# Kernel tuning notes

Measured on AMD Instinct MI355X. Metric: run time of the kernel, lower is better.

Reference implementation:

```python
import jax, jax.numpy as jnp
import numpy as np

NUM_GROUPS = 32
EPS = 1e-6


def group_norm(x, gamma, beta):
    # x: [B, C, H, W]
    B, C, H, W = x.shape
    xg = x.reshape(B, NUM_GROUPS, C // NUM_GROUPS, H, W)
    mean = jnp.mean(xg, axis=(2, 3, 4), keepdims=True)
    var = jnp.var(xg, axis=(2, 3, 4), keepdims=True)
    xn = ((xg - mean) * jax.lax.rsqrt(var + EPS)).reshape(B, C, H, W)
    return xn * gamma[None, :, None, None] + beta[None, :, None, None]


def conv1x1(x, w, b):
    # x: [B, C, H, W], w: [O, C], b: [O]  (1x1 conv == channel matmul)
    return jnp.einsum('oc,bchw->bohw', w, x) + b[None, :, None, None]


def setup_inputs() -> dict:
    key = jax.random.key(0)
    ks = jax.random.split(key, 10)
    B, C, H, W = 16, 512, 32, 32
    s = 1.0 / np.sqrt(C)
    inp = {
        'hidden_states': jax.random.normal(ks[0], (B, C, H, W), dtype=jnp.float32),
        'norm_gamma': jnp.ones((C,), dtype=jnp.float32),
        'norm_beta': jnp.zeros((C,), dtype=jnp.float32),
        'wq': jax.random.normal(ks[1], (C, C), dtype=jnp.float32) * s,
        'bq': jnp.zeros((C,), dtype=jnp.float32),
        'wk': jax.random.normal(ks[2], (C, C), dtype=jnp.float32) * s,
        'bk': jnp.zeros((C,), dtype=jnp.float32),
        'wv': jax.random.normal(ks[3], (C, C), dtype=jnp.float32) * s,
        'bv': jnp.zeros((C,), dtype=jnp.float32),
        'wo': jax.random.normal(ks[4], (C, C), dtype=jnp.float32) * s,
        'bo': jnp.zeros((C,), dtype=jnp.float32),
    }
    return inp


def reference(hidden_states, norm_gamma, norm_beta, wq, bq, wk, bk, wv, bv, wo, bo):
    residual = hidden_states
    h = group_norm(hidden_states, norm_gamma, norm_beta)
    q = conv1x1(h, wq, bq)  # [B, C, H, W]
    k = conv1x1(h, wk, bk)
    v = conv1x1(h, wv, bv)
    B, C, H, W = q.shape
    N = H * W
    qf = q.reshape(B, C, N)  # [B, C, N]
    kf = k.reshape(B, C, N)
    vf = v.reshape(B, C, N)
    scale = float(C) ** (-0.5)
    # attn_weights[b, i, j] = sum_c q[b,c,i] * k[b,c,j]
    attn = jnp.einsum('bci,bcj->bij', qf, kf) * scale
    attn = jax.nn.softmax(attn, axis=2)
    # out[b, c, i] = sum_j v[b,c,j] * attn[b,i,j]
    out = jnp.einsum('bcj,bij->bci', vf, attn).reshape(B, C, H, W)
    out = conv1x1(out, wo, bo)
    return residual + out
```

## Files before the change

kernel.cpp:

```cpp
#include <hip/hip_runtime.h>

typedef __attribute__((ext_vector_type(4))) float f32x4;
typedef __attribute__((ext_vector_type(8))) __bf16 bf16x8;
typedef __attribute__((ext_vector_type(4))) unsigned short us4;
typedef __attribute__((ext_vector_type(8))) unsigned short us8;

#define B_  16
#define C_  512
#define N_  1024
#define G_  32
#define GS  16

__device__ inline unsigned short f2bf(float f) {
  unsigned u = __builtin_bit_cast(unsigned, f);
  u += 0x7fffu + ((u >> 16) & 1u);
  return (unsigned short)(u >> 16);
}
__device__ inline float bf2f(unsigned short u) {
  unsigned x = (unsigned)u << 16;
  return __builtin_bit_cast(float, x);
}

#define GLOAD_LDS16(gp, lp) __builtin_amdgcn_global_load_lds( \
    (const __attribute__((address_space(1))) unsigned int*)(gp), \
    (__attribute__((address_space(3))) unsigned int*)(lp), 16, 0, 0)

__global__ __launch_bounds__(256) void gn_stats(const float* __restrict__ x,
                                                float* __restrict__ stats) {
  int bg = blockIdx.x;
  const float* xp = x + (long)bg * (GS * N_);
  int tid = threadIdx.x;
  float s = 0.f, ss = 0.f;
  for (int i = tid * 4; i < GS * N_; i += 1024) {
    f32x4 v = *(const f32x4*)&xp[i];
    s += v.x + v.y + v.z + v.w;
    ss += v.x * v.x + v.y * v.y + v.z * v.z + v.w * v.w;
  }
  __shared__ float r1[256], r2[256];
  r1[tid] = s; r2[tid] = ss; __syncthreads();
  for (int off = 128; off > 0; off >>= 1) {
    if (tid < off) { r1[tid] += r1[tid + off]; r2[tid] += r2[tid + off]; }
    __syncthreads();
  }
  if (tid == 0) {
    float mean = r1[0] * (1.f / (GS * N_));
    float var  = r2[0] * (1.f / (GS * N_)) - mean * mean;
    stats[bg * 2]     = mean;
    stats[bg * 2 + 1] = rsqrtf(var + 1e-6f);
  }
}

__global__ __launch_bounds__(256) void gn_apply(const float* __restrict__ x,
                                                const float* __restrict__ stats,
                                                const float* __restrict__ gamma,
                                                const float* __restrict__ beta,
                                                unsigned short* __restrict__ ht) {
  int b = blockIdx.z, ct = blockIdx.y, nt = blockIdx.x;
  int c0 = ct * 64, n0 = nt * 64;
  int tid = threadIdx.x;
  __shared__ unsigned short L[64 * 68];
  const float* xp = x + ((long)b * C_ + c0) * N_ + n0;
#pragma unroll
  for (int i = 0; i < 4; ++i) {
    int li = tid + i * 256;
    int row = li >> 4;
    int col4 = (li & 15) * 4;
    f32x4 v = *(const f32x4*)&xp[(long)row * N_ + col4];
    int c = c0 + row;
    float mean = stats[(b * G_ + (c >> 4)) * 2];
    float rstd = stats[(b * G_ + (c >> 4)) * 2 + 1];
    float gm = gamma[c] * rstd;
    float bt = beta[c] - mean * gm;
    us4 o;
    o.x = f2bf(v.x * gm + bt); o.y = f2bf(v.y * gm + bt);
    o.z = f2bf(v.z * gm + bt); o.w = f2bf(v.w * gm + bt);
    *(us4*)&L[row * 68 + col4] = o;
  }
  __syncthreads();
#pragma unroll
  for (int i = 0; i < 2; ++i) {
    int s = tid + i * 256;
    int n = s >> 3;
    int cs = (s & 7) * 8;
    us8 o;
#pragma unroll
    for (int j = 0; j < 8; ++j) o[j] = L[(cs + j) * 68 + n];
    *(us8*)&ht[((long)b * N_ + n0 + n) * C_ + c0 + cs] = o;
  }
}

__global__ __launch_bounds__(256) void convert_w(const float* __restrict__ wo,
                                                 const float* __restrict__ bv,
                                                 unsigned short* __restrict__ wob,
                                                 float* __restrict__ bvo) {
  long bid = blockIdx.x;
  int tid = threadIdx.x;
  long i = bid * 256 + tid;
  if (i < C_ * C_) wob[i] = f2bf(wo[i]);
  if (bid >= 1024) {
    int o = (int)(bid - 1024) * 256 + tid;
    const float* wr = wo + (long)o * 512;
    float acc = 0.f;
    for (int c = 0; c < 512; c += 4) {
      f32x4 w4 = *(const f32x4*)&wr[c];
      f32x4 b4 = *(const f32x4*)&bv[c];
      acc += w4.x * b4.x + w4.y * b4.y + w4.z * b4.z + w4.w * b4.w;
    }
    bvo[o] = acc;
  }
}

__global__ __launch_bounds__(256) void transpose3(const float* __restrict__ wq,
                                                  const float* __restrict__ wk,
                                                  const float* __restrict__ wv,
                                                  unsigned short* __restrict__ wqT,
                                                  unsigned short* __restrict__ wkT,
                                                  unsigned short* __restrict__ wvT) {
  const float* src = (blockIdx.z == 0) ? wq : (blockIdx.z == 1) ? wk : wv;
  unsigned short* dst = (blockIdx.z == 0) ? wqT : (blockIdx.z == 1) ? wkT : wvT;
  int c0 = blockIdx.x * 64, k0 = blockIdx.y * 64;
  int tid = threadIdx.x;
  __shared__ float Lt[64][65];
#pragma unroll
  for (int i = 0; i < 4; ++i) {
    int lin = tid + i * 256;
    int rr = lin >> 4;
    int q4 = (lin & 15) * 4;
    f32x4 v = *(const f32x4*)&src[(long)(c0 + rr) * 512 + k0 + q4];
    Lt[q4 + 0][rr] = v.x; Lt[q4 + 1][rr] = v.y;
    Lt[q4 + 2][rr] = v.z; Lt[q4 + 3][rr] = v.w;
  }
  __syncthreads();
#pragma unroll
  for (int i = 0; i < 2; ++i) {
    int lin = tid + i * 256;
    int kk = lin >> 3;
    int cc = (lin & 7) * 8;
    us8 o;
#pragma unroll
    for (int j = 0; j < 8; ++j) o[j] = f2bf(Lt[kk][cc + j]);
    *(us8*)&dst[(long)(k0 + kk) * 512 + c0 + cc] = o;
  }
}

__device__ inline f32x4 mfma16(bf16x8 a, bf16x8 b, f32x4 c) {
  return __builtin_amdgcn_mfma_f32_16x16x32_bf16(a, b, c, 0, 0, 0);
}

__global__ __launch_bounds__(256) void wprod(const unsigned short* __restrict__ wkT,
                                             const unsigned short* __restrict__ wqT,
                                             const unsigned short* __restrict__ wob,
                                             const unsigned short* __restrict__ wvT,
                                             unsigned short* __restrict__ WM,
                                             unsigned short* __restrict__ WVO) {
  const unsigned short* A = blockIdx.z ? wob : wkT;
  const unsigned short* B = blockIdx.z ? wvT : wqT;
  unsigned short* D = blockIdx.z ? WVO : WM;
  int row0 = blockIdx.x * 64, col0 = blockIdx.y * 64;
  int tid = threadIdx.x, lane = tid & 63, w = tid >> 6;
  int lr = lane & 15, kh = (lane >> 4) * 8;
  f32x4 acc4[4];
#pragma unroll
  for (int n = 0; n < 4; ++n) acc4[n] = f32x4{0.f, 0.f, 0.f, 0.f};
  for (int k0 = 0; k0 < 512; k0 += 32) {
    bf16x8 af = *(const bf16x8*)&A[(long)(row0 + w * 16 + lr) * 512 + k0 + kh];
#pragma unroll
    for (int n = 0; n < 4; ++n) {
      bf16x8 bf8 = *(const bf16x8*)&B[(long)(col0 + n * 16 + lr) * 512 + k0 + kh];
      acc4[n] = mfma16(af, bf8, acc4[n]);
    }
  }
  int rb = (lane >> 4) * 4;
#pragma unroll
  for (int n = 0; n < 4; ++n)
#pragma unroll
    for (int r = 0; r < 4; ++r)
      D[(long)(row0 + w * 16 + rb + r) * 512 + col0 + n * 16 + lr] = f2bf(acc4[n][r]);
}

__global__ __launch_bounds__(256) void uv_kernel(const unsigned short* __restrict__ wqT,
                                                 const unsigned short* __restrict__ wkT,
                                                 const float* __restrict__ bq,
                                                 const float* __restrict__ bk,
                                                 float* __restrict__ u, float* __restrict__ v,
                                                 float* __restrict__ s0g) {
  int tid = threadIdx.x, lane = tid & 63, wv_ = tid >> 6;
  int gw = blockIdx.x * 4 + wv_;
  int half = gw >> 5;
  const unsigned short* W = half ? wkT : wqT;
  const float* bvec = half ? bq : bk;
  f32x4 b4a = *(const f32x4*)&bvec[lane * 8];
  f32x4 b4b = *(const f32x4*)&bvec[lane * 8 + 4];
  for (int rr = 0; rr < 16; ++rr) {
    int row = (gw & 31) * 16 + rr;
    us8 w8 = *(const us8*)&W[(long)row * 512 + lane * 8];
    float d = bf2f(w8[0]) * b4a.x + bf2f(w8[1]) * b4a.y + bf2f(w8[2]) * b4a.z + bf2f(w8[3]) * b4a.w
            + bf2f(w8[4]) * b4b.x + bf2f(w8[5]) * b4b.y + bf2f(w8[6]) * b4b.z + bf2f(w8[7]) * b4b.w;
#pragma unroll
    for (int off = 1; off < 64; off <<= 1) d += __shfl_xor(d, off);
    if (lane == 0) { if (half) v[row] = d; else u[row] = d; }
  }
  if (gw == 0) {
    f32x4 qa = *(const f32x4*)&bq[lane * 8];
    f32x4 qb = *(const f32x4*)&bq[lane * 8 + 4];
    f32x4 ka = *(const f32x4*)&bk[lane * 8];
    f32x4 kb = *(const f32x4*)&bk[lane * 8 + 4];
    float d = qa.x * ka.x + qa.y * ka.y + qa.z * ka.z + qa.w * ka.w
            + qb.x * kb.x + qb.y * kb.y + qb.z * kb.z + qb.w * kb.w;
#pragma unroll
    for (int off = 1; off < 64; off <<= 1) d += __shfl_xor(d, off);
    if (lane == 0) s0g[0] = d;
  }
}

__global__ __launch_bounds__(256) void alphabeta(const unsigned short* __restrict__ ht,
                                                 const float* __restrict__ u,
                                                 const float* __restrict__ v,
                                                 const float* __restrict__ s0g,
                                                 float* __restrict__ alpha,
                                                 float* __restrict__ betav) {
  int tid = threadIdx.x, lane = tid & 63, w = tid >> 6;
  long gw = (long)blockIdx.x * 4 + w;
  f32x4 ua = *(const f32x4*)&u[lane * 8];
  f32x4 ub = *(const f32x4*)&u[lane * 8 + 4];
  f32x4 va = *(const f32x4*)&v[lane * 8];
  f32x4 vb = *(const f32x4*)&v[lane * 8 + 4];
  float s0 = s0g[0];
  for (int rr = 0; rr < 16; ++rr) {
    long row = gw * 16 + rr;
    us8 h8 = *(const us8*)&ht[row * 512 + lane * 8];
    float h0 = bf2f(h8[0]), h1 = bf2f(h8[1]), h2 = bf2f(h8[2]), h3 = bf2f(h8[3]);
    float h4 = bf2f(h8[4]), h5 = bf2f(h8[5]), h6 = bf2f(h8[6]), h7 = bf2f(h8[7]);
    float du = h0 * ua.x + h1 * ua.y + h2 * ua.z + h3 * ua.w
             + h4 * ub.x + h5 * ub.y + h6 * ub.z + h7 * ub.w;
    float dv = h0 * va.x + h1 * va.y + h2 * va.z + h3 * va.w
             + h4 * vb.x + h5 * vb.y + h6 * vb.z + h7 * vb.w;
#pragma unroll
    for (int off = 1; off < 64; off <<= 1) {
      du += __shfl_xor(du, off);
      dv += __shfl_xor(dv, off);
    }
    if (lane == 0) { alpha[row] = s0 + du; betav[row] = dv; }
  }
}

__device__ inline int swz(int b) { return b ^ (((b >> 9) & 1) << 5); }

template<int NREP, int EPI, int XSWZ>
__global__ __launch_bounds__(512, 2) void gemm256(
    const unsigned short* __restrict__ A, long lda, long Az,
    const unsigned short* __restrict__ Bm, long ldb, long Bz,
    void* __restrict__ Dp, long ldd, long Dz,
    const float* __restrict__ bias, float scale, int K,
    const float* __restrict__ residual, float* __restrict__ rs) {
  constexpr int BN = NREP * 64;
  int bx = blockIdx.x, by = blockIdx.y, bz = blockIdx.z;
  if constexpr (XSWZ) {
    int lin = bx + 4 * (by + 4 * bz);
    int l2  = (lin & 7) * 32 + (lin >> 3);
    bx = l2 & 3; by = (l2 >> 2) & 3; bz = l2 >> 4;
  }
  const int z = bz;
  const long row0 = (long)bx * 256;
  const long col0 = (long)by * BN;
  const int tid  = threadIdx.x;
  const int lane = tid & 63;
  const int wave = tid >> 6;
  const int wm = wave >> 2;
  const int wn = wave & 3;
  const int lr = lane & 15;
  const int khb = (lane >> 4) * 16;

  __shared__ unsigned short Abuf[2][16384];
  __shared__ unsigned short Bbuf[2][NREP * 4096];
  __shared__ float sred[256];

  const unsigned short* Ab = A  + (long)z * Az;
  const unsigned short* Bb = Bm + (long)z * Bz;

  if constexpr (EPI == 7) {
    if (tid < 256) {
      const float* rp = rs + ((long)z * 1024 + row0 + tid) * 16;
      float s = 0.f;
#pragma unroll
      for (int i = 0; i < 16; ++i) s += rp[i];
      sred[tid] = 1.f / s;
    }
    asm volatile("s_waitcnt lgkmcnt(0)" ::: "memory");
  }

  const unsigned short* gA[4];
#pragma unroll
  for (int r = 0; r < 4; ++r) {
    int L = swz(r * 8192 + tid * 16);
    gA[r] = Ab + (row0 + (L >> 7)) * lda + ((L & 127) >> 1);
  }
  const unsigned short* gB[NREP];
#pragma unroll
  for (int r = 0; r < NREP; ++r) {
    int L = swz(r * 8192 + tid * 16);
    gB[r] = Bb + (col0 + (L >> 7)) * ldb + ((L & 127) >> 1);
  }

  f32x4 acc[8][NREP];
#pragma unroll
  for (int m = 0; m < 8; ++m)
#pragma unroll
    for (int n = 0; n < NREP; ++n) acc[m][n] = f32x4{0.f, 0.f, 0.f, 0.f};

  const int NT = K >> 6;
#pragma unroll
  for (int r = 0; r < 4; ++r)    GLOAD_LDS16(gA[r], &Abuf[0][r * 4096 + wave * 512]);
#pragma unroll
  for (int r = 0; r < NREP; ++r) GLOAD_LDS16(gB[r], &Bbuf[0][r * 4096 + wave * 512]);

  for (int t = 0; t < NT; ++t) {
    int tn = t + 1; if (tn == NT) tn = 0;
    const long ko = (long)tn << 6;
    const int nb = (t + 1) & 1;
#pragma unroll
    for (int r = 0; r < 4; ++r)    GLOAD_LDS16(gA[r] + ko, &Abuf[nb][r * 4096 + wave * 512]);
#pragma unroll
    for (int r = 0; r < NREP; ++r) GLOAD_LDS16(gB[r] + ko, &Bbuf[nb][r * 4096 + wave * 512]);
    if constexpr (NREP == 4) asm volatile("s_waitcnt vmcnt(8)" ::: "memory");
    else                     asm volatile("s_waitcnt vmcnt(6)" ::: "memory");
    __builtin_amdgcn_s_barrier();
    __builtin_amdgcn_sched_barrier(0);
    const unsigned short* Al = Abuf[t & 1];
    const unsigned short* Bl = Bbuf[t & 1];
#pragma unroll
    for (int kk = 0; kk < 2; ++kk) {
      bf16x8 af[8], bfr[NREP];
#pragma unroll
      for (int m = 0; m < 8; ++m) {
        int Pb = swz((wm * 128 + m * 16 + lr) * 128 + kk * 64 + khb);
        af[m] = *(const bf16x8*)((const char*)Al + Pb);
      }
#pragma unroll
      for (int n = 0; n < NREP; ++n) {
        int Pb = swz((wn * (NREP * 16) + n * 16 + lr) * 128 + kk * 64 + khb);
        bfr[n] = *(const bf16x8*)((const char*)Bl + Pb);
      }
      __builtin_amdgcn_s_setprio(1);
#pragma unroll
      for (int m = 0; m < 8; ++m)
#pragma unroll
        for (int n = 0; n < NREP; ++n)
          acc[m][n] = mfma16(af[m], bfr[n], acc[m][n]);
      __builtin_amdgcn_s_setprio(0);
    }
    __builtin_amdgcn_sched_barrier(0);
    __builtin_amdgcn_s_barrier();
    __builtin_amdgcn_sched_barrier(0);
  }
  asm volatile("s_waitcnt vmcnt(0)" ::: "memory");
  __builtin_amdgcn_s_barrier();

  const int rb = (lane >> 4) * 4;

  if constexpr (EPI == 7) {
#pragma unroll
    for (int m = 0; m < 8; ++m) {
      int lrow = wm * 128 + m * 16 + rb;
      long gr0 = row0 + lrow;
#pragma unroll
      for (int n = 0; n < NREP; ++n) {
        long gc = col0 + wn * (NREP * 16) + n * 16 + lr;
        long o = (long)z * (512L * 1024L) + gc * 1024L + gr0;
        f32x4 res = *(const f32x4*)&residual[o];
        float bb = bias[gc];
        f32x4 st;
#pragma unroll
        for (int r = 0; r < 4; ++r)
          st[r] = acc[m][n][r] * sred[lrow + r] + bb + res[r];
        *(f32x4*)&((float*)Dp)[o] = st;
      }
    }
    return;
  }

  float* slab = ((float*)(void*)Abuf) + wave * 1088;
  const int jt = by;
  unsigned short* Dst = (unsigned short*)Dp + (long)z * Dz;
  float bc[NREP];
  if constexpr (EPI == 5) {
#pragma unroll
    for (int n = 0; n < NREP; ++n)
      bc[n] = residual[(long)z * 1024 + col0 + wn * (NREP * 16) + n * 16 + lr];
  }
#pragma unroll
  for (int m = 0; m < 8; ++m) {
    float ps[4] = {0.f, 0.f, 0.f, 0.f};
    float ar[4];
    if constexpr (EPI == 5) {
#pragma unroll
      for (int r = 0; r < 4; ++r)
        ar[r] = bias[(long)z * 1024 + row0 + wm * 128 + m * 16 + rb + r];
    }
#pragma unroll
    for (int n = 0; n < NREP; ++n) {
#pragma unroll
      for (int r = 0; r < 4; ++r) {
        float v = acc[m][n][r];
        if constexpr (EPI == 1) v += bias[row0 + wm * 128 + m * 16 + rb + r];
        else if constexpr (EPI == 5) { v = exp2f((v + ar[r] + bc[n]) * scale); ps[r] += v; }
        slab[(rb + r) * 68 + n * 16 + lr] = v;
      }
    }
    if constexpr (EPI == 5) {
#pragma unroll
      for (int r = 0; r < 4; ++r) {
        ps[r] += __shfl_xor(ps[r], 1);
        ps[r] += __shfl_xor(ps[r], 2);
        ps[r] += __shfl_xor(ps[r], 4);
        ps[r] += __shfl_xor(ps[r], 8);
      }
      if (lr == 0) {
#pragma unroll
        for (int r = 0; r < 4; ++r)
          rs[((long)z * 1024 + row0 + wm * 128 + m * 16 + rb + r) * 16 + jt * 4 + wn] = ps[r];
      }
    }
    if constexpr (NREP == 4) {
#pragma unroll
      for (int p = 0; p < 2; ++p) {
        int rl = p * 8 + (lane >> 3);
        int c8 = (lane & 7) * 8;
        f32x4 v0 = *(const f32x4*)&slab[rl * 68 + c8];
        f32x4 v1 = *(const f32x4*)&slab[rl * 68 + c8 + 4];
        us8 o;
        o[0] = f2bf(v0.x); o[1] = f2bf(v0.y); o[2] = f2bf(v0.z); o[3] = f2bf(v0.w);
        o[4] = f2bf(v1.x); o[5] = f2bf(v1.y); o[6] = f2bf(v1.z); o[7] = f2bf(v1.w);
        *(us8*)&Dst[(row0 + wm * 128 + m * 16 + rl) * ldd + col0 + wn * 64 + c8] = o;
      }
    } else {
      int rl = lane >> 2;
      int c8 = (lane & 3) * 8;
      f32x4 v0 = *(const f32x4*)&slab[rl * 68 + c8];
      f32x4 v1 = *(const f32x4*)&slab[rl * 68 + c8 + 4];
      us8 o;
      o[0] = f2bf(v0.x); o[1] = f2bf(v0.y); o[2] = f2bf(v0.z); o[3] = f2bf(v0.w);
      o[4] = f2bf(v1.x); o[5] = f2bf(v1.y); o[6] = f2bf(v1.z); o[7] = f2bf(v1.w);
      *(us8*)&Dst[(row0 + wm * 128 + m * 16 + rl) * ldd + col0 + wn * 32 + c8] = o;
    }
  }
}

extern "C" void kernel_launch(void* const* d_in, const int* in_sizes, int n_in,
                              void* d_out, int out_size, void* d_ws, size_t ws_size,
                              hipStream_t stream) {
  const float* x     = (const float*)d_in[0];
  const float* gamma = (const float*)d_in[1];
  const float* beta  = (const float*)d_in[2];
  const float* wq    = (const float*)d_in[3];
  const float* bq    = (const float*)d_in[4];
  const float* wk    = (const float*)d_in[5];
  const float* bk    = (const float*)d_in[6];
  const float* wv    = (const float*)d_in[7];
  const float* bv    = (const float*)d_in[8];
  const float* wo    = (const float*)d_in[9];
  const float* bo    = (const float*)d_in[10];
  float* out = (float*)d_out;

  char* ws = (char*)d_ws;
  unsigned short* ht   = (unsigned short*)(ws + 0);
  unsigned short* T    = (unsigned short*)(ws + 16777216);
  unsigned short* VWT  = (unsigned short*)(ws + 33554432);
  unsigned short* S    = (unsigned short*)(ws + 50331648);
  unsigned short* wqT  = (unsigned short*)(ws + 83886080);
  unsigned short* wkT  = (unsigned short*)(ws + 84410368);
  unsigned short* wvT  = (unsigned short*)(ws + 84934656);
  unsigned short* wob  = (unsigned short*)(ws + 85458944);
  unsigned short* WM   = (unsigned short*)(ws + 85983232);
  unsigned short* WVO  = (unsigned short*)(ws + 86507520);
  float* u             = (float*)(ws + 87031808);
  float* v             = (float*)(ws + 87033856);
  float* s0g           = (float*)(ws + 87035904);
  float* bvo           = (float*)(ws + 87037952);
  float* stats         = (float*)(ws + 87040000);
  float* alpha         = (float*)(ws + 87046144);
  float* betav         = (float*)(ws + 87111680);
  float* rs            = (float*)(ws + 87177216);

  convert_w<<<1026, 256, 0, stream>>>(wo, bv, wob, bvo);
  transpose3<<<dim3(8, 8, 3), 256, 0, stream>>>(wq, wk, wv, wqT, wkT, wvT);
  wprod<<<dim3(8, 8, 2), 256, 0, stream>>>(wkT, wqT, wob, wvT, WM, WVO);
  uv_kernel<<<16, 256, 0, stream>>>(wqT, wkT, bq, bk, u, v, s0g);
  gn_stats<<<512, 256, 0, stream>>>(x, stats);
  gn_apply<<<dim3(16, 8, 16), 256, 0, stream>>>(x, stats, gamma, beta, ht);
  alphabeta<<<256, 256, 0, stream>>>(ht, u, v, s0g, alpha, betav);

  gemm256<2, 3, 0><<<dim3(64, 4, 1), 512, 0, stream>>>(ht, 512, 0, WM, 512, 0,
                                                       T, 512, 0, nullptr, 0.f, 512, nullptr, nullptr);
  gemm256<2, 1, 0><<<dim3(2, 128, 1), 512, 0, stream>>>(WVO, 512, 0, ht, 512, 0,
                                                        VWT, 16384, 0, bvo, 0.f, 512, nullptr, nullptr);
  gemm256<4, 5, 1><<<dim3(4, 4, 16), 512, 0, stream>>>(T, 512, 524288L, ht, 512, 524288L,
                                                       S, 1024, 1048576L, alpha,
                                                       0.06375871416f, 512, betav, rs);
  gemm256<2, 7, 1><<<dim3(4, 4, 16), 512, 0, stream>>>(S, 1024, 1048576L,
                                                       VWT, 16384, 1024,
                                                       out, 0, 0, bo, 0.f, 1024, x, rs);
}
```

Before: 166.3 us.

## Fuse group-norm stats and apply; shrink GEMM tiles to 128x128 for more blocks

Merges the group-norm statistics and apply kernels into one kernel that stages each group's slice in LDS, so x is read once instead of twice and one launch is removed. All GEMMs switch from 256-row, 512-thread tiles to 128x128 tiles with 256 threads, and the grid swizzle is generalized. This quadruples block counts (e.g. 256 to 1024 for the score GEMM) to fill more CUs, at the cost of less data reuse per tile and more global/L2 traffic. The row-sum partial layout changes to match the new tiling.

```diff
diff --git a/kernel.cpp b/kernel.cpp
--- a/kernel.cpp
+++ b/kernel.cpp
@@ -25,67 +25,49 @@
     (const __attribute__((address_space(1))) unsigned int*)(gp), \
     (__attribute__((address_space(3))) unsigned int*)(lp), 16, 0, 0)
 
-__global__ __launch_bounds__(256) void gn_stats(const float* __restrict__ x,
-                                                float* __restrict__ stats) {
+__global__ __launch_bounds__(256) void gn_fused(const float* __restrict__ x,
+                                                const float* __restrict__ gamma,
+                                                const float* __restrict__ beta,
+                                                unsigned short* __restrict__ ht) {
   int bg = blockIdx.x;
-  const float* xp = x + (long)bg * (GS * N_);
+  int b = bg >> 5, g = bg & 31;
   int tid = threadIdx.x;
+  __shared__ float Lx[16][1028];
+  __shared__ float r1[256], r2[256];
+  const float* xp = x + ((long)b * C_ + g * 16) * N_;
   float s = 0.f, ss = 0.f;
-  for (int i = tid * 4; i < GS * N_; i += 1024) {
-    f32x4 v = *(const f32x4*)&xp[i];
-    s += v.x + v.y + v.z + v.w;
+#pragma unroll
+  for (int i = 0; i < 16; ++i) {
+    f32x4 v = *(const f32x4*)&xp[(long)i * N_ + tid * 4];
+    s  += v.x + v.y + v.z + v.w;
     ss += v.x * v.x + v.y * v.y + v.z * v.z + v.w * v.w;
-  }
-  __shared__ float r1[256], r2[256];
+    *(f32x4*)&Lx[i][tid * 4] = v;
+  }
   r1[tid] = s; r2[tid] = ss; __syncthreads();
   for (int off = 128; off > 0; off >>= 1) {
     if (tid < off) { r1[tid] += r1[tid + off]; r2[tid] += r2[tid + off]; }
     __syncthreads();
   }
-  if (tid == 0) {
-    float mean = r1[0] * (1.f / (GS * N_));
-    float var  = r2[0] * (1.f / (GS * N_)) - mean * mean;
-    stats[bg * 2]     = mean;
-    stats[bg * 2 + 1] = rsqrtf(var + 1e-6f);
-  }
-}
-
-__global__ __launch_bounds__(256) void gn_apply(const float* __restrict__ x,
-                                                const float* __restrict__ stats,
-                                                const float* __restrict__ gamma,
-                                                const float* __restrict__ beta,
-                                                unsigned short* __restrict__ ht) {
-  int b = blockIdx.z, ct = blockIdx.y, nt = blockIdx.x;
-  int c0 = ct * 64, n0 = nt * 64;
-  int tid = threadIdx.x;
-  __shared__ unsigned short L[64 * 68];
-  const float* xp = x + ((long)b * C_ + c0) * N_ + n0;
-#pragma unroll
-  for (int i = 0; i < 4; ++i) {
-    int li = tid + i * 256;
-    int row = li >> 4;
-    int col4 = (li & 15) * 4;
-    f32x4 v = *(const f32x4*)&xp[(long)row * N_ + col4];
-    int c = c0 + row;
-    float mean = stats[(b * G_ + (c >> 4)) * 2];
-    float rstd = stats[(b * G_ + (c >> 4)) * 2 + 1];
-    float gm = gamma[c] * rstd;
-    float bt = beta[c] - mean * gm;
-    us4 o;
-    o.x = f2bf(v.x * gm + bt); o.y = f2bf(v.y * gm + bt);
-    o.z = f2bf(v.z * gm + bt); o.w = f2bf(v.w * gm + bt);
-    *(us4*)&L[row * 68 + col4] = o;
-  }
-  __syncthreads();
-#pragma unroll
-  for (int i = 0; i < 2; ++i) {
-    int s = tid + i * 256;
-    int n = s >> 3;
-    int cs = (s & 7) * 8;
+  float mean = r1[0] * (1.f / 16384.f);
+  float var  = r2[0] * (1.f / 16384.f) - mean * mean;
+  float rstd = rsqrtf(var + 1e-6f);
+  float gm[8], bt[8];
+  int cbase = g * 16 + (tid & 1) * 8;
+#pragma unroll
+  for (int k = 0; k < 8; ++k) {
+    gm[k] = gamma[cbase + k] * rstd;
+    bt[k] = beta[cbase + k] - mean * gm[k];
+  }
+#pragma unroll
+  for (int j = 0; j < 8; ++j) {
+    int lin = tid + j * 256;
+    int n = lin >> 1;
+    int c8 = (lin & 1) * 8;
     us8 o;
 #pragma unroll
-    for (int j = 0; j < 8; ++j) o[j] = L[(cs + j) * 68 + n];
-    *(us8*)&ht[((long)b * N_ + n0 + n) * C_ + c0 + cs] = o;
+    for (int k = 0; k < 8; ++k)
+      o[k] = f2bf(Lx[c8 + k][n] * gm[k] + bt[k]);
+    *(us8*)&ht[((long)b * N_ + n) * C_ + g * 16 + c8] = o;
   }
 }
 
@@ -246,40 +228,42 @@
 
 __device__ inline int swz(int b) { return b ^ (((b >> 9) & 1) << 5); }
 
-template<int NREP, int EPI, int XSWZ>
-__global__ __launch_bounds__(512, 2) void gemm256(
+template<int EPI, int SHX, int SHY, int XSWZ>
+__global__ __launch_bounds__(256, 2) void gemm128(
     const unsigned short* __restrict__ A, long lda, long Az,
     const unsigned short* __restrict__ Bm, long ldb, long Bz,
     void* __restrict__ Dp, long ldd, long Dz,
     const float* __restrict__ bias, float scale, int K,
     const float* __restrict__ residual, float* __restrict__ rs) {
-  constexpr int BN = NREP * 64;
   int bx = blockIdx.x, by = blockIdx.y, bz = blockIdx.z;
   if constexpr (XSWZ) {
-    int lin = bx + 4 * (by + 4 * bz);
-    int l2  = (lin & 7) * 32 + (lin >> 3);
-    bx = l2 & 3; by = (l2 >> 2) & 3; bz = l2 >> 4;
+    int lin = bx + ((by + (bz << SHY)) << SHX);
+    int cpx = 1 << (SHX + SHY + 4 - 3);
+    int l2  = (lin & 7) * cpx + (lin >> 3);
+    bx = l2 & ((1 << SHX) - 1);
+    by = (l2 >> SHX) & ((1 << SHY) - 1);
+    bz = l2 >> (SHX + SHY);
   }
   const int z = bz;
-  const long row0 = (long)bx * 256;
-  const long col0 = (long)by * BN;
+  const long row0 = (long)bx * 128;
+  const long col0 = (long)by * 128;
   const int tid  = threadIdx.x;
   const int lane = tid & 63;
   const int wave = tid >> 6;
-  const int wm = wave >> 2;
-  const int wn = wave & 3;
+  const int wm = wave >> 1;
+  const int wn = wave & 1;
   const int lr = lane & 15;
   const int khb = (lane >> 4) * 16;
 
-  __shared__ unsigned short Abuf[2][16384];
-  __shared__ unsigned short Bbuf[2][NREP * 4096];
-  __shared__ float sred[256];
+  __shared__ unsigned short Abuf[2][8192];
+  __shared__ unsigned short Bbuf[2][8192];
+  __shared__ float sred[128];
 
   const unsigned short* Ab = A  + (long)z * Az;
   const unsigned short* Bb = Bm + (long)z * Bz;
 
   if constexpr (EPI == 7) {
-    if (tid < 256) {
+    if (tid < 128) {
       const float* rp = rs + ((long)z * 1024 + row0 + tid) * 16;
       float s = 0.f;
 #pragma unroll
@@ -290,62 +274,61 @@
   }
 
   const unsigned short* gA[4];
+  const unsigned short* gB[4];
 #pragma unroll
   for (int r = 0; r < 4; ++r) {
-    int L = swz(r * 8192 + tid * 16);
+    int L = swz(r * 4096 + tid * 16);
     gA[r] = Ab + (row0 + (L >> 7)) * lda + ((L & 127) >> 1);
-  }
-  const unsigned short* gB[NREP];
-#pragma unroll
-  for (int r = 0; r < NREP; ++r) {
-    int L = swz(r * 8192 + tid * 16);
     gB[r] = Bb + (col0 + (L >> 7)) * ldb + ((L & 127) >> 1);
   }
 
-  f32x4 acc[8][NREP];
-#pragma unroll
-  for (int m = 0; m < 8; ++m)
-#pragma unroll
-    for (int n = 0; n < NREP; ++n) acc[m][n] = f32x4{0.f, 0.f, 0.f, 0.f};
+  f32x4 acc[4][4];
+#pragma unroll
+  for (int m = 0; m < 4; ++m)
+#pragma unroll
+    for (int n = 0; n < 4; ++n) acc[m][n] = f32x4{0.f, 0.f, 0.f, 0.f};
 
   const int NT = K >> 6;
-#pragma unroll
-  for (int r = 0; r < 4; ++r)    GLOAD_LDS16(gA[r], &Abuf[0][r * 4096 + wave * 512]);
-#pragma unroll
-  for (int r = 0; r < NREP; ++r) GLOAD_LDS16(gB[r], &Bbuf[0][r * 4096 + wave * 512]);
+  const int ldsO = wave * 512;
+
+#pragma unroll
+  for (int r = 0; r < 4; ++r) {
+    GLOAD_LDS16(gA[r], &Abuf[0][r * 2048 + ldsO]);
+    GLOAD_LDS16(gB[r], &Bbuf[0][r * 2048 + ldsO]);
+  }
 
   for (int t = 0; t < NT; ++t) {
     int tn = t + 1; if (tn == NT) tn = 0;
     const long ko = (long)tn << 6;
     const int nb = (t + 1) & 1;
 #pragma unroll
-    for (int r = 0; r < 4; ++r)    GLOAD_LDS16(gA[r] + ko, &Abuf[nb][r * 4096 + wave * 512]);
-#pragma unroll
-    for (int r = 0; r < NREP; ++r) GLOAD_LDS16(gB[r] + ko, &Bbuf[nb][r * 4096 + wave * 512]);
-    if constexpr (NREP == 4) asm volatile("s_waitcnt vmcnt(8)" ::: "memory");
-    else                     asm volatile("s_waitcnt vmcnt(6)" ::: "memory");
+    for (int r = 0; r < 4; ++r) {
+      GLOAD_LDS16(gA[r] + ko, &Abuf[nb][r * 2048 + ldsO]);
+      GLOAD_LDS16(gB[r] + ko, &Bbuf[nb][r * 2048 + ldsO]);
+    }
+    asm volatile("s_waitcnt vmcnt(8)" ::: "memory");
     __builtin_amdgcn_s_barrier();
     __builtin_amdgcn_sched_barrier(0);
     const unsigned short* Al = Abuf[t & 1];
     const unsigned short* Bl = Bbuf[t & 1];
 #pragma unroll
     for (int kk = 0; kk < 2; ++kk) {
-      bf16x8 af[8], bfr[NREP];
-#pragma unroll
-      for (int m = 0; m < 8; ++m) {
-        int Pb = swz((wm * 128 + m * 16 + lr) * 128 + kk * 64 + khb);
+      bf16x8 af[4], bfr[4];
+#pragma unroll
+      for (int m = 0; m < 4; ++m) {
+        int Pb = swz((wm * 64 + m * 16 + lr) * 128 + kk * 64 + khb);
         af[m] = *(const bf16x8*)((const char*)Al + Pb);
       }
 #pragma unroll
-      for (int n = 0; n < NREP; ++n) {
-        int Pb = swz((wn * (NREP * 16) + n * 16 + lr) * 128 + kk * 64 + khb);
+      for (int n = 0; n < 4; ++n) {
+        int Pb = swz((wn * 64 + n * 16 + lr) * 128 + kk * 64 + khb);
         bfr[n] = *(const bf16x8*)((const char*)Bl + Pb);
       }
       __builtin_amdgcn_s_setprio(1);
 #pragma unroll
-      for (int m = 0; m < 8; ++m)
-#pragma unroll
-        for (int n = 0; n < NREP; ++n)
+      for (int m = 0; m < 4; ++m)
+#pragma unroll
+        for (int n = 0; n < 4; ++n)
           acc[m][n] = mfma16(af[m], bfr[n], acc[m][n]);
       __builtin_amdgcn_s_setprio(0);
     }
@@ -360,12 +343,12 @@
 
   if constexpr (EPI == 7) {
 #pragma unroll
-    for (int m = 0; m < 8; ++m) {
-      int lrow = wm * 128 + m * 16 + rb;
+    for (int m = 0; m < 4; ++m) {
+      int lrow = wm * 64 + m * 16 + rb;
       long gr0 = row0 + lrow;
 #pragma unroll
-      for (int n = 0; n < NREP; ++n) {
-        long gc = col0 + wn * (NREP * 16) + n * 16 + lr;
+      for (int n = 0; n < 4; ++n) {
+        long gc = col0 + wn * 64 + n * 16 + lr;
         long o = (long)z * (512L * 1024L) + gc * 1024L + gr0;
         f32x4 res = *(const f32x4*)&residual[o];
         float bb = bias[gc];
@@ -382,27 +365,27 @@
   float* slab = ((float*)(void*)Abuf) + wave * 1088;
   const int jt = by;
   unsigned short* Dst = (unsigned short*)Dp + (long)z * Dz;
-  float bc[NREP];
+  float bc[4];
   if constexpr (EPI == 5) {
 #pragma unroll
-    for (int n = 0; n < NREP; ++n)
-      bc[n] = residual[(long)z * 1024 + col0 + wn * (NREP * 16) + n * 16 + lr];
-  }
-#pragma unroll
-  for (int m = 0; m < 8; ++m) {
+    for (int n = 0; n < 4; ++n)
+      bc[n] = residual[(long)z * 1024 + col0 + wn * 64 + n * 16 + lr];
+  }
+#pragma unroll
+  for (int m = 0; m < 4; ++m) {
     float ps[4] = {0.f, 0.f, 0.f, 0.f};
     float ar[4];
     if constexpr (EPI == 5) {
 #pragma unroll
       for (int r = 0; r < 4; ++r)
-        ar[r] = bias[(long)z * 1024 + row0 + wm * 128 + m * 16 + rb + r];
-    }
-#pragma unroll
-    for (int n = 0; n < NREP; ++n) {
+        ar[r] = bias[(long)z * 1024 + row0 + wm * 64 + m * 16 + rb + r];
+    }
+#pragma unroll
+    for (int n = 0; n < 4; ++n) {
 #pragma unroll
       for (int r = 0; r < 4; ++r) {
         float v = acc[m][n][r];
-        if constexpr (EPI == 1) v += bias[row0 + wm * 128 + m * 16 + rb + r];
+        if constexpr (EPI == 1) v += bias[row0 + wm * 64 + m * 16 + rb + r];
         else if constexpr (EPI == 5) { v = exp2f((v + ar[r] + bc[n]) * scale); ps[r] += v; }
         slab[(rb + r) * 68 + n * 16 + lr] = v;
       }
@@ -418,30 +401,19 @@
       if (lr == 0) {
 #pragma unroll
         for (int r = 0; r < 4; ++r)
-          rs[((long)z * 1024 + row0 + wm * 128 + m * 16 + rb + r) * 16 + jt * 4 + wn] = ps[r];
-      }
-    }
-    if constexpr (NREP == 4) {
-#pragma unroll
-      for (int p = 0; p < 2; ++p) {
-        int rl = p * 8 + (lane >> 3);
-        int c8 = (lane & 7) * 8;
-        f32x4 v0 = *(const f32x4*)&slab[rl * 68 + c8];
-        f32x4 v1 = *(const f32x4*)&slab[rl * 68 + c8 + 4];
-        us8 o;
-        o[0] = f2bf(v0.x); o[1] = f2bf(v0.y); o[2] = f2bf(v0.z); o[3] = f2bf(v0.w);
-        o[4] = f2bf(v1.x); o[5] = f2bf(v1.y); o[6] = f2bf(v1.z); o[7] = f2bf(v1.w);
-        *(us8*)&Dst[(row0 + wm * 128 + m * 16 + rl) * ldd + col0 + wn * 64 + c8] = o;
-      }
-    } else {
-      int rl = lane >> 2;
-      int c8 = (lane & 3) * 8;
+          rs[((long)z * 1024 + row0 + wm * 64 + m * 16 + rb + r) * 16 + jt * 2 + wn] = ps[r];
+      }
+    }
+#pragma unroll
+    for (int p = 0; p < 2; ++p) {
+      int rl = p * 8 + (lane >> 3);
+      int c8 = (lane & 7) * 8;
       f32x4 v0 = *(const f32x4*)&slab[rl * 68 + c8];
       f32x4 v1 = *(const f32x4*)&slab[rl * 68 + c8 + 4];
       us8 o;
       o[0] = f2bf(v0.x); o[1] = f2bf(v0.y); o[2] = f2bf(v0.z); o[3] = f2bf(v0.w);
       o[4] = f2bf(v1.x); o[5] = f2bf(v1.y); o[6] = f2bf(v1.z); o[7] = f2bf(v1.w);
-      *(us8*)&Dst[(row0 + wm * 128 + m * 16 + rl) * ldd + col0 + wn * 32 + c8] = o;
+      *(us8*)&Dst[(row0 + wm * 64 + m * 16 + rl) * ldd + col0 + wn * 64 + c8] = o;
     }
   }
 }
@@ -477,7 +449,6 @@
   float* v             = (float*)(ws + 87033856);
   float* s0g           = (float*)(ws + 87035904);
   float* bvo           = (float*)(ws + 87037952);
-  float* stats         = (float*)(ws + 87040000);
   float* alpha         = (float*)(ws + 87046144);
   float* betav         = (float*)(ws + 87111680);
   float* rs            = (float*)(ws + 87177216);
@@ -486,18 +457,17 @@
   transpose3<<<dim3(8, 8, 3), 256, 0, stream>>>(wq, wk, wv, wqT, wkT, wvT);
   wprod<<<dim3(8, 8, 2), 256, 0, stream>>>(wkT, wqT, wob, wvT, WM, WVO);
   uv_kernel<<<16, 256, 0, stream>>>(wqT, wkT, bq, bk, u, v, s0g);
-  gn_stats<<<512, 256, 0, stream>>>(x, stats);
-  gn_apply<<<dim3(16, 8, 16), 256, 0, stream>>>(x, stats, gamma, beta, ht);
+  gn_fused<<<512, 256, 0, stream>>>(x, gamma, beta, ht);
   alphabeta<<<256, 256, 0, stream>>>(ht, u, v, s0g, alpha, betav);
 
-  gemm256<2, 3, 0><<<dim3(64, 4, 1), 512, 0, stream>>>(ht, 512, 0, WM, 512, 0,
-                                                       T, 512, 0, nullptr, 0.f, 512, nullptr, nullptr);
-  gemm256<2, 1, 0><<<dim3(2, 128, 1), 512, 0, stream>>>(WVO, 512, 0, ht, 512, 0,
-                                                        VWT, 16384, 0, bvo, 0.f, 512, nullptr, nullptr);
-  gemm256<4, 5, 1><<<dim3(4, 4, 16), 512, 0, stream>>>(T, 512, 524288L, ht, 512, 524288L,
-                                                       S, 1024, 1048576L, alpha,
-                                                       0.06375871416f, 512, betav, rs);
-  gemm256<2, 7, 1><<<dim3(4, 4, 16), 512, 0, stream>>>(S, 1024, 1048576L,
-                                                       VWT, 16384, 1024,
-                                                       out, 0, 0, bo, 0.f, 1024, x, rs);
-}
+  gemm128<3, 0, 0, 0><<<dim3(128, 4, 1), 256, 0, stream>>>(ht, 512, 0, WM, 512, 0,
+                                                           T, 512, 0, nullptr, 0.f, 512, nullptr, nullptr);
+  gemm128<1, 0, 0, 0><<<dim3(4, 128, 1), 256, 0, stream>>>(WVO, 512, 0, ht, 512, 0,
+                                                           VWT, 16384, 0, bvo, 0.f, 512, nullptr, nullptr);
+  gemm128<5, 3, 3, 1><<<dim3(8, 8, 16), 256, 0, stream>>>(T, 512, 524288L, ht, 512, 524288L,
+                                                          S, 1024, 1048576L, alpha,
+                                                          0.06375871416f, 512, betav, rs);
+  gemm128<7, 3, 2, 1><<<dim3(8, 4, 16), 256, 0, stream>>>(S, 1024, 1048576L,
+                                                          VWT, 16384, 1024,
+                                                          out, 0, 0, bo, 0.f, 1024, x, rs);
+}
```

New measurement: 154.3 us. 7.2% less time.
